# Kernel tuning notes

Measured on AMD Instinct MI355X. Metric: run time of the kernel, lower is better.

Reference implementation:

```python
import jax, jax.numpy as jnp
import numpy as np

ALPHA = 0.2      # LeakyReLU negative slope
NEG_INF = -9e15  # mask value from the original code

def setup_inputs() -> dict:
    key = jax.random.key(0)
    k1, k2, k3, k4 = jax.random.split(key, 4)
    B, M, F_IN, F_OUT = 16, 2048, 128, 64
    h = jax.random.normal(k1, (B, M, F_IN), dtype=jnp.float32)
    adj = jax.random.randint(k2, (B, M, M), 0, 2, dtype=jnp.int32)
    W = jax.random.normal(k3, (F_IN, F_OUT), dtype=jnp.float32) * 0.1
    a = jax.random.normal(k4, (2 * F_OUT, 1), dtype=jnp.float32) * 0.1
    return {"h": h, "adj": adj, "W": W, "a": a}

def reference(h, adj, W, a):
    # h: [B,M,Fin], adj: [B,M,M], W: [Fin,E], a: [2E,1]
    Wh = jnp.matmul(h, W)                      # [B,M,E]
    E = Wh.shape[-1]
    a1, a2 = a[:E, 0], a[E:, 0]
    # decompose a^T [Wh_i || Wh_j] = (Wh_i . a1) + (Wh_j . a2)
    f1 = Wh @ a1                               # [B,M] (source/query term)
    f2 = Wh @ a2                               # [B,M] (target/key term)
    e = jax.nn.leaky_relu(f1[:, :, None] + f2[:, None, :], negative_slope=ALPHA)  # [B,M,M]
    scores = jnp.where(adj > 0, e, NEG_INF)
    attn = jax.nn.softmax(scores, axis=-1)     # [B,M,M]  (dropout p=0 / eval mode)
    h_prime = jnp.matmul(attn, Wh)             # [B,M,E]
    return jax.nn.elu(h_prime)                 # concat=True branch
```

## Files before the change

### kernel.cpp

```cpp
#include <hip/hip_runtime.h>


#define M_     2048
#define FIN_   128
#define F_     64
#define ALPHA_ 0.2f
#define ROWS_  32
#define TS_    36
#define WT_    132

typedef float  float4_ __attribute__((ext_vector_type(4)));
typedef short  short4_ __attribute__((ext_vector_type(4)));
typedef short  short8  __attribute__((ext_vector_type(8)));
typedef int    int4_   __attribute__((ext_vector_type(4)));
typedef unsigned short u16;
typedef unsigned int   u32;

static __device__ __forceinline__ float bf2f(u16 u) {
    return __uint_as_float(((u32)u) << 16);
}
static __device__ __forceinline__ u16 f2bf(float f) {
    u32 u = __float_as_uint(f);
    u32 r = u + 0x7FFFu + ((u >> 16) & 1u);
    return (u16)(r >> 16);
}

__global__ __launch_bounds__(256, 4) void k_gat2(
    const float* __restrict__ h, const int* __restrict__ adj,
    const float* __restrict__ W, const float* __restrict__ a,
    float* __restrict__ out)
{
    __shared__ u16   Wl[FIN_ * F_];
    __shared__ float a_s[2 * F_];
    __shared__ float wa1[FIN_], wa2[FIN_];
    __shared__ float f1s[ROWS_];
    __shared__ float dens[ROWS_];
    __shared__ char  dyn[32 * WT_ * 4];

    u16*   hT   = (u16*)dyn;
    u16*   P    = (u16*)(dyn + 9216);
    float* f2t  = (float*)(dyn + 11520);
    float* Tsum = (float*)dyn;

    const int tid  = threadIdx.x;
    const int w    = tid >> 6;
    const int l    = tid & 63;
    const int lc   = l & 15;
    const int quad = l >> 4;
    const int b    = blockIdx.x >> 6;
    const int i0   = (blockIdx.x & 63) * ROWS_;

    if (tid < 128) a_s[tid] = a[tid];
    for (int e = tid; e < FIN_ * F_; e += 256) Wl[e] = f2bf(W[e]);
    __syncthreads();

    if (tid < FIN_) {
        float s1 = 0.f, s2 = 0.f;
#pragma unroll 8
        for (int n = 0; n < F_; ++n) {
            float wv = W[tid * F_ + n];
            s1 += wv * a_s[n];
            s2 += wv * a_s[F_ + n];
        }
        wa1[tid] = s1;
        wa2[tid] = s2;
    }
    __syncthreads();

    {
        const int i = tid >> 3, sub = tid & 7, k0 = sub * 16;
        const float* hp = h + ((size_t)(b * M_ + i0 + i)) * FIN_ + k0;
        float s = 0.f;
#pragma unroll
        for (int k = 0; k < 16; ++k) s += hp[k] * wa1[k0 + k];
        s += __shfl_xor(s, 1, 64);
        s += __shfl_xor(s, 2, 64);
        s += __shfl_xor(s, 4, 64);
        if (sub == 0) f1s[i] = s;
    }
    __syncthreads();

    const int prow = tid >> 3;
    const int ps   = tid & 7;
    const int sf0  = (tid & 15) * 8;
    const int stp  = (tid >> 4) * 2;
    const int mt   = w & 1;
    const int ntb  = (w >> 1) * 4;
    const float f1r = f1s[prow];
    float denacc = 0.f;

    float4_ acc[4];
#pragma unroll
    for (int c = 0; c < 4; ++c) acc[c] = (float4_){0.f, 0.f, 0.f, 0.f};

    const int*   aprow = adj + ((size_t)(b * M_ + i0 + prow)) * M_ + ps * 4;
    const float* hbase = h + ((size_t)(b * M_ + stp)) * FIN_ + sf0;

    for (int it = 0; it < 64; ++it) {
        const int j0 = it * 32;

        int4_ c4 = *(const int4_*)(aprow + j0);

        {
            const float* hp0 = hbase + (size_t)j0 * FIN_;
            const float* hp1 = hp0 + FIN_;
            float4_ x0 = *(const float4_*)hp0, x1 = *(const float4_*)(hp0 + 4);
            float4_ y0 = *(const float4_*)hp1, y1 = *(const float4_*)(hp1 + 4);
            float xa[8] = {x0[0], x0[1], x0[2], x0[3], x1[0], x1[1], x1[2], x1[3]};
            float ya[8] = {y0[0], y0[1], y0[2], y0[3], y1[0], y1[1], y1[2], y1[3]};
            float fp0 = 0.f, fp1 = 0.f;
#pragma unroll
            for (int kk = 0; kk < 8; ++kk) {
                const int k = sf0 + kk;
                u16 u0 = f2bf(xa[kk]), u1 = f2bf(ya[kk]);
                *(u32*)(hT + k * TS_ + stp) = (u32)u0 | ((u32)u1 << 16);
                fp0 += xa[kk] * wa2[k];
                fp1 += ya[kk] * wa2[k];
            }
            fp0 += __shfl_xor(fp0, 1, 64); fp1 += __shfl_xor(fp1, 1, 64);
            fp0 += __shfl_xor(fp0, 2, 64); fp1 += __shfl_xor(fp1, 2, 64);
            fp0 += __shfl_xor(fp0, 4, 64); fp1 += __shfl_xor(fp1, 4, 64);
            fp0 += __shfl_xor(fp0, 8, 64); fp1 += __shfl_xor(fp1, 8, 64);
            if ((tid & 15) == 0) { f2t[stp] = fp0; f2t[stp + 1] = fp1; }
        }
        __syncthreads();

        {
            float4_ g = *(const float4_*)(f2t + ps * 4);
            u32 pk0, pk1;
            float d = 0.f;
            {
                float x_ = f1r + g[0]; x_ = fmaxf(x_, ALPHA_ * x_);
                float e_ = (c4[0] > 0) ? __expf(x_) : 0.f;
                u16 pb = f2bf(e_); d += bf2f(pb); pk0 = (u32)pb;
            }
            {
                float x_ = f1r + g[1]; x_ = fmaxf(x_, ALPHA_ * x_);
                float e_ = (c4[1] > 0) ? __expf(x_) : 0.f;
                u16 pb = f2bf(e_); d += bf2f(pb); pk0 |= ((u32)pb << 16);
            }
            {
                float x_ = f1r + g[2]; x_ = fmaxf(x_, ALPHA_ * x_);
                float e_ = (c4[2] > 0) ? __expf(x_) : 0.f;
                u16 pb = f2bf(e_); d += bf2f(pb); pk1 = (u32)pb;
            }
            {
                float x_ = f1r + g[3]; x_ = fmaxf(x_, ALPHA_ * x_);
                float e_ = (c4[3] > 0) ? __expf(x_) : 0.f;
                u16 pb = f2bf(e_); d += bf2f(pb); pk1 |= ((u32)pb << 16);
            }
            *(u32*)(P + prow * TS_ + ps * 4)     = pk0;
            *(u32*)(P + prow * TS_ + ps * 4 + 2) = pk1;
            denacc += d;
        }
        __syncthreads();

        {
            const u16* apx = P + (mt * 16 + lc) * TS_ + quad * 8;
            short4_ a0 = *(const short4_*)apx;
            short4_ a1 = *(const short4_*)(apx + 4);
            short8 af;
            af[0] = a0[0]; af[1] = a0[1]; af[2] = a0[2]; af[3] = a0[3];
            af[4] = a1[0]; af[5] = a1[1]; af[6] = a1[2]; af[7] = a1[3];
#pragma unroll
            for (int c = 0; c < 4; ++c) {
                const u16* bp = hT + ((ntb + c) * 16 + lc) * TS_ + quad * 8;
                short4_ b0 = *(const short4_*)bp;
                short4_ b1 = *(const short4_*)(bp + 4);
                short8 bf;
                bf[0] = b0[0]; bf[1] = b0[1]; bf[2] = b0[2]; bf[3] = b0[3];
                bf[4] = b1[0]; bf[5] = b1[1]; bf[6] = b1[2]; bf[7] = b1[3];
                acc[c] = __builtin_amdgcn_mfma_f32_16x16x32_bf16(af, bf, acc[c], 0, 0, 0);
            }
        }
        __syncthreads();
    }

    denacc += __shfl_xor(denacc, 1, 64);
    denacc += __shfl_xor(denacc, 2, 64);
    denacc += __shfl_xor(denacc, 4, 64);
    if (ps == 0) dens[prow] = denacc;

#pragma unroll
    for (int c = 0; c < 4; ++c)
#pragma unroll
        for (int mm = 0; mm < 4; ++mm)
            Tsum[(mt * 16 + quad * 4 + mm) * WT_ + (ntb + c) * 16 + lc] = acc[c][mm];
    __syncthreads();

    {
        const int row = tid >> 3;
        const int n0  = (tid & 7) * 8;
        const float den  = dens[row];
        const float rden = (den > 0.f) ? (1.f / den) : 0.f;
        float u[8];
#pragma unroll
        for (int nn = 0; nn < 8; ++nn) u[nn] = 0.f;
        for (int k = 0; k < FIN_; ++k) {
            const float tv = Tsum[row * WT_ + k];
            const u16* wp = &Wl[k * F_ + n0];
#pragma unroll
            for (int nn = 0; nn < 8; ++nn) u[nn] += tv * bf2f(wp[nn]);
        }
        float4_ o0, o1;
#pragma unroll
        for (int nn = 0; nn < 8; ++nn) {
            float hp = u[nn] * rden;
            float o  = hp > 0.f ? hp : expm1f(hp);
            if (nn < 4) o0[nn] = o; else o1[nn - 4] = o;
        }
        float* op = out + ((size_t)(b * M_ + i0 + row)) * F_ + n0;
        *(float4_*)op       = o0;
        *(float4_*)(op + 4) = o1;
    }
}

extern "C" void kernel_launch(void* const* d_in, const int* in_sizes, int n_in,
                              void* d_out, int out_size, void* d_ws, size_t ws_size,
                              hipStream_t stream)
{
    (void)out_size; (void)d_ws; (void)ws_size;
    const float* h  = (const float*)d_in[0];
    const int* adjp = (const int*)d_in[1];
    const float* Wp = (const float*)d_in[2];
    const float* ap = (const float*)d_in[3];
    for (int i = 0; i < n_in; ++i) {
        long s = in_sizes[i];
        if      (s == 4194304L)  h    = (const float*)d_in[i];
        else if (s == 67108864L) adjp = (const int*)d_in[i];
        else if (s == 8192L)     Wp   = (const float*)d_in[i];
        else if (s == 128L)      ap   = (const float*)d_in[i];
    }
    k_gat2<<<1024, 256, 0, stream>>>(h, adjp, Wp, ap, (float*)d_out);
}
```

Measured before the change: 434.7 us.

## Double-buffer hT tile, prefetch adj/h, compute scores in MFMA registers, 64-row blocks

Each block now covers 64 query rows with 512 threads, so every h tile staged in shared memory serves twice as many rows. f2 for all keys is computed up front instead of per tile. The inner loop double-buffers the transposed h tile and prefetches adj rows two tiles ahead and h one tile ahead into registers, which brings it down to one barrier per iteration. Attention probabilities go straight into the MFMA A-operand registers rather than through a shared P buffer, and the hT stores are XOR-swizzled to reduce bank conflicts. In exchange the kernel uses more registers and shared memory, and only 512 blocks are launched, which may lower occupancy.

Result: slower. 449.1 us (+3.3%).

```diff
diff --git a/kernel.cpp b/kernel.cpp
--- a/kernel.cpp
+++ b/kernel.cpp
@@ -5,7 +5,7 @@
 #define FIN_   128
 #define F_     64
 #define ALPHA_ 0.2f
-#define ROWS_  32
+#define ROWS_  64
 #define TS_    36
 #define WT_    132
 
@@ -25,7 +25,7 @@
     return (u16)(r >> 16);
 }
 
-__global__ __launch_bounds__(256, 4) void k_gat2(
+__global__ __launch_bounds__(512, 4) void k_gat3(
     const float* __restrict__ h, const int* __restrict__ adj,
     const float* __restrict__ W, const float* __restrict__ a,
     float* __restrict__ out)
@@ -35,23 +35,23 @@
     __shared__ float wa1[FIN_], wa2[FIN_];
     __shared__ float f1s[ROWS_];
     __shared__ float dens[ROWS_];
-    __shared__ char  dyn[32 * WT_ * 4];
-
-    u16*   hT   = (u16*)dyn;
-    u16*   P    = (u16*)(dyn + 9216);
-    float* f2t  = (float*)(dyn + 11520);
-    float* Tsum = (float*)dyn;
+    __shared__ char  dyn[WT_ * 64 * 4];
+
+    u16*   hTbuf0 = (u16*)dyn;
+    u16*   hTbuf1 = (u16*)(dyn + 9216);
+    float* f2all  = (float*)(dyn + 18432);
+    float* Tsum   = (float*)dyn;
 
     const int tid  = threadIdx.x;
     const int w    = tid >> 6;
     const int l    = tid & 63;
     const int lc   = l & 15;
     const int quad = l >> 4;
-    const int b    = blockIdx.x >> 6;
-    const int i0   = (blockIdx.x & 63) * ROWS_;
+    const int b    = blockIdx.x >> 5;
+    const int i0   = (blockIdx.x & 31) * ROWS_;
 
     if (tid < 128) a_s[tid] = a[tid];
-    for (int e = tid; e < FIN_ * F_; e += 256) Wl[e] = f2bf(W[e]);
+    for (int e = tid; e < FIN_ * F_; e += 512) Wl[e] = f2bf(W[e]);
     __syncthreads();
 
     if (tid < FIN_) {
@@ -68,139 +68,150 @@
     __syncthreads();
 
     {
-        const int i = tid >> 3, sub = tid & 7, k0 = sub * 16;
-        const float* hp = h + ((size_t)(b * M_ + i0 + i)) * FIN_ + k0;
+        const int r = tid >> 3, k0 = (tid & 7) * 16;
+        const float* hp = h + ((size_t)(b * M_ + i0 + r)) * FIN_ + k0;
         float s = 0.f;
 #pragma unroll
         for (int k = 0; k < 16; ++k) s += hp[k] * wa1[k0 + k];
         s += __shfl_xor(s, 1, 64);
         s += __shfl_xor(s, 2, 64);
         s += __shfl_xor(s, 4, 64);
-        if (sub == 0) f1s[i] = s;
-    }
-    __syncthreads();
-
-    const int prow = tid >> 3;
-    const int ps   = tid & 7;
-    const int sf0  = (tid & 15) * 8;
-    const int stp  = (tid >> 4) * 2;
-    const int mt   = w & 1;
-    const int ntb  = (w >> 1) * 4;
-    const float f1r = f1s[prow];
+        if ((tid & 7) == 0) f1s[r] = s;
+    }
+
+    {
+        const int sf0 = (tid & 15) * 8;
+        for (int p = 0; p < 64; ++p) {
+            const int t = p * 32 + (tid >> 4);
+            const float* hp = h + ((size_t)(b * M_ + t)) * FIN_ + sf0;
+            float4_ x0 = *(const float4_*)hp;
+            float4_ x1 = *(const float4_*)(hp + 4);
+            float fp = 0.f;
+            fp += x0[0] * wa2[sf0 + 0]; fp += x0[1] * wa2[sf0 + 1];
+            fp += x0[2] * wa2[sf0 + 2]; fp += x0[3] * wa2[sf0 + 3];
+            fp += x1[0] * wa2[sf0 + 4]; fp += x1[1] * wa2[sf0 + 5];
+            fp += x1[2] * wa2[sf0 + 6]; fp += x1[3] * wa2[sf0 + 7];
+            fp += __shfl_xor(fp, 1, 64);
+            fp += __shfl_xor(fp, 2, 64);
+            fp += __shfl_xor(fp, 4, 64);
+            fp += __shfl_xor(fp, 8, 64);
+            if ((tid & 15) == 0) f2all[t] = fp;
+        }
+    }
+
+    const int rg  = w & 3;
+    const int nh  = w >> 2;
+    const int tq  = tid >> 5;
+    const int f0  = (tid & 31) * 4;
+    const int row = i0 + rg * 16 + lc;
+
+    const int*   aprow  = adj + ((size_t)(b * M_ + row)) * M_ + quad * 8;
+    const float* hstage = h + ((size_t)(b * M_ + 2 * tq)) * FIN_ + f0;
+
+    int4_   aA0 = *(const int4_*)(aprow);
+    int4_   aA1 = *(const int4_*)(aprow + 4);
+    int4_   aB0 = *(const int4_*)(aprow + 32);
+    int4_   aB1 = *(const int4_*)(aprow + 36);
+    float4_ hA0 = *(const float4_*)(hstage);
+    float4_ hA1 = *(const float4_*)(hstage + FIN_);
+
+    __syncthreads();
+
+    const float f1r = f1s[rg * 16 + lc];
     float denacc = 0.f;
-
-    float4_ acc[4];
-#pragma unroll
-    for (int c = 0; c < 4; ++c) acc[c] = (float4_){0.f, 0.f, 0.f, 0.f};
-
-    const int*   aprow = adj + ((size_t)(b * M_ + i0 + prow)) * M_ + ps * 4;
-    const float* hbase = h + ((size_t)(b * M_ + stp)) * FIN_ + sf0;
-
-    for (int it = 0; it < 64; ++it) {
-        const int j0 = it * 32;
-
-        int4_ c4 = *(const int4_*)(aprow + j0);
-
-        {
-            const float* hp0 = hbase + (size_t)j0 * FIN_;
-            const float* hp1 = hp0 + FIN_;
-            float4_ x0 = *(const float4_*)hp0, x1 = *(const float4_*)(hp0 + 4);
-            float4_ y0 = *(const float4_*)hp1, y1 = *(const float4_*)(hp1 + 4);
-            float xa[8] = {x0[0], x0[1], x0[2], x0[3], x1[0], x1[1], x1[2], x1[3]};
-            float ya[8] = {y0[0], y0[1], y0[2], y0[3], y1[0], y1[1], y1[2], y1[3]};
-            float fp0 = 0.f, fp1 = 0.f;
-#pragma unroll
-            for (int kk = 0; kk < 8; ++kk) {
-                const int k = sf0 + kk;
-                u16 u0 = f2bf(xa[kk]), u1 = f2bf(ya[kk]);
-                *(u32*)(hT + k * TS_ + stp) = (u32)u0 | ((u32)u1 << 16);
-                fp0 += xa[kk] * wa2[k];
-                fp1 += ya[kk] * wa2[k];
-            }
-            fp0 += __shfl_xor(fp0, 1, 64); fp1 += __shfl_xor(fp1, 1, 64);
-            fp0 += __shfl_xor(fp0, 2, 64); fp1 += __shfl_xor(fp1, 2, 64);
-            fp0 += __shfl_xor(fp0, 4, 64); fp1 += __shfl_xor(fp1, 4, 64);
-            fp0 += __shfl_xor(fp0, 8, 64); fp1 += __shfl_xor(fp1, 8, 64);
-            if ((tid & 15) == 0) { f2t[stp] = fp0; f2t[stp + 1] = fp1; }
-        }
-        __syncthreads();
-
-        {
-            float4_ g = *(const float4_*)(f2t + ps * 4);
-            u32 pk0, pk1;
-            float d = 0.f;
-            {
-                float x_ = f1r + g[0]; x_ = fmaxf(x_, ALPHA_ * x_);
-                float e_ = (c4[0] > 0) ? __expf(x_) : 0.f;
-                u16 pb = f2bf(e_); d += bf2f(pb); pk0 = (u32)pb;
-            }
-            {
-                float x_ = f1r + g[1]; x_ = fmaxf(x_, ALPHA_ * x_);
-                float e_ = (c4[1] > 0) ? __expf(x_) : 0.f;
-                u16 pb = f2bf(e_); d += bf2f(pb); pk0 |= ((u32)pb << 16);
-            }
-            {
-                float x_ = f1r + g[2]; x_ = fmaxf(x_, ALPHA_ * x_);
-                float e_ = (c4[2] > 0) ? __expf(x_) : 0.f;
-                u16 pb = f2bf(e_); d += bf2f(pb); pk1 = (u32)pb;
-            }
-            {
-                float x_ = f1r + g[3]; x_ = fmaxf(x_, ALPHA_ * x_);
-                float e_ = (c4[3] > 0) ? __expf(x_) : 0.f;
-                u16 pb = f2bf(e_); d += bf2f(pb); pk1 |= ((u32)pb << 16);
-            }
-            *(u32*)(P + prow * TS_ + ps * 4)     = pk0;
-            *(u32*)(P + prow * TS_ + ps * 4 + 2) = pk1;
-            denacc += d;
-        }
-        __syncthreads();
-
-        {
-            const u16* apx = P + (mt * 16 + lc) * TS_ + quad * 8;
-            short4_ a0 = *(const short4_*)apx;
-            short4_ a1 = *(const short4_*)(apx + 4);
-            short8 af;
-            af[0] = a0[0]; af[1] = a0[1]; af[2] = a0[2]; af[3] = a0[3];
-            af[4] = a1[0]; af[5] = a1[1]; af[6] = a1[2]; af[7] = a1[3];
-#pragma unroll
-            for (int c = 0; c < 4; ++c) {
-                const u16* bp = hT + ((ntb + c) * 16 + lc) * TS_ + quad * 8;
-                short4_ b0 = *(const short4_*)bp;
-                short4_ b1 = *(const short4_*)(bp + 4);
-                short8 bf;
-                bf[0] = b0[0]; bf[1] = b0[1]; bf[2] = b0[2]; bf[3] = b0[3];
-                bf[4] = b1[0]; bf[5] = b1[1]; bf[6] = b1[2]; bf[7] = b1[3];
-                acc[c] = __builtin_amdgcn_mfma_f32_16x16x32_bf16(af, bf, acc[c], 0, 0, 0);
-            }
-        }
-        __syncthreads();
-    }
-
-    denacc += __shfl_xor(denacc, 1, 64);
-    denacc += __shfl_xor(denacc, 2, 64);
-    denacc += __shfl_xor(denacc, 4, 64);
-    if (ps == 0) dens[prow] = denacc;
-
-#pragma unroll
-    for (int c = 0; c < 4; ++c)
-#pragma unroll
-        for (int mm = 0; mm < 4; ++mm)
-            Tsum[(mt * 16 + quad * 4 + mm) * WT_ + (ntb + c) * 16 + lc] = acc[c][mm];
+    float4_ acc0 = {0.f,0.f,0.f,0.f}, acc1 = {0.f,0.f,0.f,0.f};
+    float4_ acc2 = {0.f,0.f,0.f,0.f}, acc3 = {0.f,0.f,0.f,0.f};
+
+    for (int t = 0; t < 64; ++t) {
+        u16* hT = (t & 1) ? hTbuf1 : hTbuf0;
+        const int j0 = t * 32;
+        const int jn = (t < 63 ? t + 1 : 63) * 32;
+        const int jp = (t < 62 ? t + 2 : 63) * 32;
+
+        int4_   aC0 = *(const int4_*)(aprow + jp);
+        int4_   aC1 = *(const int4_*)(aprow + jp + 4);
+        float4_ hN0 = *(const float4_*)(hstage + (size_t)jn * FIN_);
+        float4_ hN1 = *(const float4_*)(hstage + (size_t)jn * FIN_ + FIN_);
+
+#pragma unroll
+        for (int kk = 0; kk < 4; ++kk) {
+            const int k   = f0 + kk;
+            const int swz = (k >> 3) & 12;
+            u32 pk = (u32)f2bf(hA0[kk]) | ((u32)f2bf(hA1[kk]) << 16);
+            *(u32*)(hT + k * TS_ + 2 * (tq ^ swz)) = pk;
+        }
+
+        asm volatile("s_waitcnt lgkmcnt(0)" ::: "memory");
+        __builtin_amdgcn_s_barrier();
+        __builtin_amdgcn_sched_barrier(0);
+
+        float4_ g0 = *(const float4_*)(f2all + j0 + quad * 8);
+        float4_ g1 = *(const float4_*)(f2all + j0 + quad * 8 + 4);
+        short8 af;
+        float d = 0.f;
+#define SCORE(J, GV, AV)                                   \
+        {                                                  \
+            float x_ = f1r + (GV);                         \
+            x_ = fmaxf(x_, ALPHA_ * x_);                   \
+            float e_ = ((AV) > 0) ? __expf(x_) : 0.f;      \
+            u16 pb = f2bf(e_);                             \
+            d += bf2f(pb);                                 \
+            af[J] = (short)pb;                             \
+        }
+        SCORE(0, g0[0], aA0[0]) SCORE(1, g0[1], aA0[1])
+        SCORE(2, g0[2], aA0[2]) SCORE(3, g0[3], aA0[3])
+        SCORE(4, g1[0], aA1[0]) SCORE(5, g1[1], aA1[1])
+        SCORE(6, g1[2], aA1[2]) SCORE(7, g1[3], aA1[3])
+#undef SCORE
+        denacc += d;
+
+#define MTILE(C, ACC)                                                        \
+        {                                                                    \
+            const int fidx = (nh * 4 + (C)) * 16 + lc;                       \
+            const int swzf = ((nh * 4 + (C)) * 2) & 12;                      \
+            const u16* bp = hT + fidx * TS_ + (((quad * 4) ^ swzf) << 1);    \
+            short4_ b0 = *(const short4_*)bp;                                \
+            short4_ b1 = *(const short4_*)(bp + 4);                          \
+            short8 bf;                                                       \
+            bf[0] = b0[0]; bf[1] = b0[1]; bf[2] = b0[2]; bf[3] = b0[3];      \
+            bf[4] = b1[0]; bf[5] = b1[1]; bf[6] = b1[2]; bf[7] = b1[3];      \
+            ACC = __builtin_amdgcn_mfma_f32_16x16x32_bf16(af, bf, ACC, 0, 0, 0); \
+        }
+        MTILE(0, acc0) MTILE(1, acc1) MTILE(2, acc2) MTILE(3, acc3)
+#undef MTILE
+
+        aA0 = aB0; aA1 = aB1; aB0 = aC0; aB1 = aC1;
+        hA0 = hN0; hA1 = hN1;
+    }
+
+    denacc += __shfl_xor(denacc, 16, 64);
+    denacc += __shfl_xor(denacc, 32, 64);
+    if (nh == 0 && quad == 0) dens[rg * 16 + lc] = denacc;
+    __syncthreads();
+
+#pragma unroll
+    for (int mm = 0; mm < 4; ++mm) {
+        const int rr = (rg * 16 + quad * 4 + mm) * WT_ + nh * 64 + lc;
+        Tsum[rr +  0] = acc0[mm];
+        Tsum[rr + 16] = acc1[mm];
+        Tsum[rr + 32] = acc2[mm];
+        Tsum[rr + 48] = acc3[mm];
+    }
     __syncthreads();
 
     {
-        const int row = tid >> 3;
-        const int n0  = (tid & 7) * 8;
-        const float den  = dens[row];
+        const int r  = tid >> 3;
+        const int n0 = (tid & 7) * 8;
+        const float den  = dens[r];
         const float rden = (den > 0.f) ? (1.f / den) : 0.f;
         float u[8];
 #pragma unroll
         for (int nn = 0; nn < 8; ++nn) u[nn] = 0.f;
         for (int k = 0; k < FIN_; ++k) {
-            const float tv = Tsum[row * WT_ + k];
-            const u16* wp = &Wl[k * F_ + n0];
-#pragma unroll
-            for (int nn = 0; nn < 8; ++nn) u[nn] += tv * bf2f(wp[nn]);
+            const float tv = Tsum[r * WT_ + k];
+            short8 wv = *(const short8*)(Wl + k * F_ + n0);
+#pragma unroll
+            for (int nn = 0; nn < 8; ++nn) u[nn] += tv * bf2f((u16)wv[nn]);
         }
         float4_ o0, o1;
 #pragma unroll
@@ -209,7 +220,7 @@
             float o  = hp > 0.f ? hp : expm1f(hp);
             if (nn < 4) o0[nn] = o; else o1[nn - 4] = o;
         }
-        float* op = out + ((size_t)(b * M_ + i0 + row)) * F_ + n0;
+        float* op = out + ((size_t)(b * M_ + i0 + r)) * F_ + n0;
         *(float4_*)op       = o0;
         *(float4_*)(op + 4) = o1;
     }
@@ -231,5 +242,5 @@
         else if (s == 8192L)     Wp   = (const float*)d_in[i];
         else if (s == 128L)      ap   = (const float*)d_in[i];
     }
-    k_gat2<<<1024, 256, 0, stream>>>(h, adjp, Wp, ap, (float*)d_out);
-}
+    k_gat3<<<512, 512, 0, stream>>>(h, adjp, Wp, ap, (float*)d_out);
+}
```
